# Performance work log

Measured on AMD Instinct MI355X. Metric: run time of the kernel, lower is better.

Reference implementation:

```python
import jax, jax.numpy as jnp
import numpy as np

GROUPS = 8
EPS = 1e-3  # keras GroupNormalization default epsilon


def group_norm(x, gamma, beta):
    # x: [B, H, W, C], channels-last, normalize over (H, W, C//G) per group
    B, H, W, C = x.shape
    g = x.reshape(B, H, W, GROUPS, C // GROUPS)
    mean = g.mean(axis=(1, 2, 4), keepdims=True)
    var = g.var(axis=(1, 2, 4), keepdims=True)
    g = (g - mean) * jax.lax.rsqrt(var + EPS)
    return g.reshape(B, H, W, C) * gamma + beta


def setup_inputs() -> dict:
    key = jax.random.key(0)
    ks = jax.random.split(key, 6)
    B, H, W, C = 4, 64, 64, 256
    s = 1.0 / np.sqrt(C)
    return {
        "x": jax.random.normal(ks[0], (B, H, W, C), jnp.float32),
        "gn_gamma": jnp.ones((C,), jnp.float32),
        "gn_beta": jnp.zeros((C,), jnp.float32),
        "Wq": jax.random.normal(ks[1], (C, C), jnp.float32) * s,
        "bq": jnp.zeros((C,), jnp.float32),
        "Wk": jax.random.normal(ks[2], (C, C), jnp.float32) * s,
        "bk": jnp.zeros((C,), jnp.float32),
        "Wv": jax.random.normal(ks[3], (C, C), jnp.float32) * s,
        "bv": jnp.zeros((C,), jnp.float32),
        "Wp": jax.random.normal(ks[4], (C, C), jnp.float32) * s,
        "bp": jnp.zeros((C,), jnp.float32),
    }


def reference(x, gn_gamma, gn_beta, Wq, bq, Wk, bk, Wv, bv, Wp, bp):
    B, H, W, C = x.shape
    scale = jnp.float32(C) ** -0.5
    xn = group_norm(x, gn_gamma, gn_beta)  # note: residual uses NORMALIZED input (as in source)
    xf = xn.reshape(B, H * W, C)           # flatten spatial -> [B, N, C]
    q = xf @ Wq + bq
    k = xf @ Wk + bk
    v = xf @ Wv + bv
    attn = jnp.einsum('bnc,bmc->bnm', q, k) * scale  # [B, N, N]
    attn = jax.nn.softmax(attn, axis=-1)
    out = jnp.einsum('bnm,bmc->bnc', attn, v)
    out = out @ Wp + bp
    return xn + out.reshape(B, H, W, C)
```

## Files before the change

kernel.cpp:

```cpp
#include <hip/hip_runtime.h>
#include <hip/hip_bf16.h>

typedef __bf16 bf16x8 __attribute__((ext_vector_type(8)));
typedef __bf16 bf16x4 __attribute__((ext_vector_type(4)));
typedef float f32x4 __attribute__((ext_vector_type(4)));
typedef float f32x16 __attribute__((ext_vector_type(16)));

#define MFMA16(a,b,c) __builtin_amdgcn_mfma_f32_16x16x32_bf16((a),(b),(c),0,0,0)
#define MFMA32(a,b,c) __builtin_amdgcn_mfma_f32_32x32x16_bf16((a),(b),(c),0,0,0)

__device__ __forceinline__ void gload_lds16(const void* g, void* l) {
    __builtin_amdgcn_global_load_lds((const __attribute__((address_space(1))) unsigned int*)g,
                                     (__attribute__((address_space(3))) unsigned int*)l, 16, 0, 0);
}

__global__ __launch_bounds__(256) void gn_stats1(const float* __restrict__ x,
                                                 float* __restrict__ pstats) {
    int blk = blockIdx.x;
    int bg = blk >> 4, sl = blk & 15;
    int b = bg >> 3, g = bg & 7;
    const float* base = x + ((size_t)b * 4096 + sl * 256) * 256 + g * 32;
    float s = 0.f, s2 = 0.f;
    for (int i = threadIdx.x; i < 2048; i += 256) {
        int pos = i >> 3, f4 = i & 7;
        float4 v = *(const float4*)(base + (size_t)pos * 256 + f4 * 4);
        s  += v.x + v.y + v.z + v.w;
        s2 += v.x * v.x + v.y * v.y + v.z * v.z + v.w * v.w;
    }
    for (int off = 32; off; off >>= 1) {
        s  += __shfl_down(s, off);
        s2 += __shfl_down(s2, off);
    }
    __shared__ float red[8];
    int wave = threadIdx.x >> 6, lane = threadIdx.x & 63;
    if (lane == 0) { red[wave] = s; red[4 + wave] = s2; }
    __syncthreads();
    if (threadIdx.x == 0) {
        pstats[blk * 2]     = red[0] + red[1] + red[2] + red[3];
        pstats[blk * 2 + 1] = red[4] + red[5] + red[6] + red[7];
    }
}

__global__ void gn_stats2(const float* __restrict__ pstats, float* __restrict__ stats) {
    int bg = threadIdx.x;
    if (bg < 32) {
        float S = 0.f, S2 = 0.f;
        for (int sl = 0; sl < 16; sl++) {
            S  += pstats[(bg * 16 + sl) * 2];
            S2 += pstats[(bg * 16 + sl) * 2 + 1];
        }
        const float invN = 1.f / 131072.f;
        float mean = S * invN;
        float var = S2 * invN - mean * mean;
        stats[bg * 2] = mean;
        stats[bg * 2 + 1] = rsqrtf(var + 1e-3f);
    }
}

__global__ __launch_bounds__(256) void gn_norm(const float* __restrict__ x,
                                               const float* __restrict__ gamma,
                                               const float* __restrict__ beta,
                                               const float* __restrict__ stats,
                                               float* __restrict__ xn_f32,
                                               __bf16* __restrict__ xn_bf) {
    size_t idx = (size_t)blockIdx.x * 256 + threadIdx.x;
    int c4 = (int)(idx & 63);
    int row = (int)(idx >> 6);
    int b = row >> 12;
    int g = c4 >> 3;
    float mean = stats[(b * 8 + g) * 2];
    float rstd = stats[(b * 8 + g) * 2 + 1];
    float4 xv = ((const float4*)x)[idx];
    float4 ga = ((const float4*)gamma)[c4];
    float4 be = ((const float4*)beta)[c4];
    float4 r;
    r.x = (xv.x - mean) * rstd * ga.x + be.x;
    r.y = (xv.y - mean) * rstd * ga.y + be.y;
    r.z = (xv.z - mean) * rstd * ga.z + be.z;
    r.w = (xv.w - mean) * rstd * ga.w + be.w;
    ((float4*)xn_f32)[idx] = r;
    bf16x4 o;
    o[0] = (__bf16)r.x; o[1] = (__bf16)r.y; o[2] = (__bf16)r.z; o[3] = (__bf16)r.w;
    *(bf16x4*)(xn_bf + idx * 4) = o;
}

__global__ __launch_bounds__(256) void prep_w(const float* __restrict__ Wq,
                                              const float* __restrict__ Wk,
                                              const float* __restrict__ Wv,
                                              const float* __restrict__ Wp,
                                              __bf16* __restrict__ wt) {
    int o = blockIdx.x * 256 + threadIdx.x;
    int w = o >> 16;
    int rem = o & 65535;
    int nt   = rem >> 12;
    int kf   = (rem >> 9) & 7;
    int quad = (rem >> 7) & 3;
    int l16  = (rem >> 3) & 15;
    int j    = rem & 7;
    int n = nt * 16 + l16;
    int k = kf * 32 + quad * 8 + j;
    const float* W = (w == 0) ? Wq : (w == 1) ? Wk : (w == 2) ? Wv : Wp;
    wt[o] = (__bf16)W[k * 256 + n];
}

__global__ __launch_bounds__(128, 2) void qkv_gemm(const __bf16* __restrict__ xn,
                                                   const __bf16* __restrict__ wt,
                                                   const float* __restrict__ bq,
                                                   const float* __restrict__ bk,
                                                   const float* __restrict__ bv,
                                                   __bf16* __restrict__ qout,
                                                   __bf16* __restrict__ kout,
                                                   __bf16* __restrict__ vtout) {
    __shared__ __bf16 atile[64][264];
    int w = blockIdx.z;
    const __bf16* Wl = wt + (size_t)w * 65536;
    int tid = threadIdx.x;
    int wave = tid >> 6, lane = tid & 63;
    int quad = lane >> 4, l16 = lane & 15;
    int m0 = blockIdx.x * 64;
    int ntbase = blockIdx.y * 8 + wave * 4;

#pragma unroll
    for (int i = 0; i < 16; i++) {
        int c = tid + 128 * i;
        int row = c >> 5, col = (c & 31) * 8;
        *(bf16x8*)&atile[row][col] = *(const bf16x8*)(xn + (size_t)(m0 + row) * 256 + col);
    }
    bf16x8 bfr[4][8];
#pragma unroll
    for (int ct = 0; ct < 4; ct++)
#pragma unroll
        for (int kf = 0; kf < 8; kf++)
            bfr[ct][kf] = *(const bf16x8*)(Wl + ((((size_t)(ntbase + ct) * 8 + kf) * 4 + quad) * 16 + l16) * 8);
    __syncthreads();

    f32x4 acc[4][4];
#pragma unroll
    for (int mt = 0; mt < 4; mt++)
#pragma unroll
        for (int ct = 0; ct < 4; ct++)
#pragma unroll
            for (int r = 0; r < 4; r++) acc[mt][ct][r] = 0.f;
#pragma unroll
    for (int kf = 0; kf < 8; kf++) {
        bf16x8 af[4];
#pragma unroll
        for (int mt = 0; mt < 4; mt++)
            af[mt] = *(const bf16x8*)&atile[mt * 16 + l16][kf * 32 + quad * 8];
#pragma unroll
        for (int mt = 0; mt < 4; mt++)
#pragma unroll
            for (int ct = 0; ct < 4; ct++)
                acc[mt][ct] = MFMA16(af[mt], bfr[ct][kf], acc[mt][ct]);
    }

    if (w == 2) {
        __syncthreads();
        __bf16 (*vtl)[70] = (__bf16(*)[70])atile;
#pragma unroll
        for (int mt = 0; mt < 4; mt++) {
#pragma unroll
            for (int ct = 0; ct < 4; ct++) {
                int cl = (wave * 4 + ct) * 16 + l16;
                float bias_v = bv[blockIdx.y * 128 + cl];
                bf16x4 pv;
#pragma unroll
                for (int r = 0; r < 4; r++) pv[r] = (__bf16)(acc[mt][ct][r] + bias_v);
                *(bf16x4*)&vtl[cl][mt * 16 + quad * 4] = pv;
            }
        }
        __syncthreads();
        int bb = m0 >> 12, n0g = m0 & 4095;
#pragma unroll
        for (int j = 0; j < 8; j++) {
            int chunk = tid + 128 * j;
            int cl = chunk >> 3, n8 = chunk & 7;
            *(bf16x8*)(vtout + ((size_t)(bb * 256 + blockIdx.y * 128 + cl)) * 4096 + n0g + n8 * 8)
                = *(const bf16x8*)&vtl[cl][n8 * 8];
        }
    } else {
        const float* bias = (w == 0) ? bq : bk;
        const float qscale = 0.09016844f;
#pragma unroll
        for (int mt = 0; mt < 4; mt++) {
#pragma unroll
            for (int ct = 0; ct < 4; ct++) {
                int c = (ntbase + ct) * 16 + l16;
                float bias_v = bias[c];
#pragma unroll
                for (int r = 0; r < 4; r++) {
                    int m = m0 + mt * 16 + quad * 4 + r;
                    float val = acc[mt][ct][r] + bias_v;
                    if (w == 0) qout[(size_t)m * 256 + c] = (__bf16)(val * qscale);
                    else        kout[(size_t)m * 256 + c] = (__bf16)val;
                }
            }
        }
    }
}

__global__ __launch_bounds__(256, 2) void flash_attn(const __bf16* __restrict__ q,
                                                     const __bf16* __restrict__ k,
                                                     const __bf16* __restrict__ vt,
                                                     __bf16* __restrict__ po,
                                                     float* __restrict__ ml) {
    __shared__ __align__(16) char smem[69632];
    __bf16 (*vtile0)[36] = (__bf16(*)[36])(smem + 32768);
    __bf16 (*vtile1)[36] = (__bf16(*)[36])(smem + 51200);
    __bf16 (*otr)[32][264] = (__bf16(*)[32][264])smem;

    const int tid = threadIdx.x;
    const int wave = tid >> 6, lane = tid & 63;
    const int l32 = lane & 31, h = lane >> 5;
    const int fid = blockIdx.x;
    const int cid = ((fid & 7) << 6) | (fid >> 3);
    const int qt  = cid & 31;
    const int ksb = cid >> 5;
    const int ks  = ksb & 3, b = ksb >> 2;
    const int row0 = qt * 128 + wave * 32;
    const size_t rowg0 = (size_t)b * 4096 + row0;

    const char*   kb = (const char*)(k + ((size_t)b * 4096 + ks * 1024) * 256);
    const __bf16* vb = vt + (size_t)b * 256 * 4096 + ks * 1024;

    int koff[4];
#pragma unroll
    for (int i = 0; i < 4; i++) {
        int P = wave * 256 + i * 64 + lane;
        int r = P >> 5, cp = P & 31;
        koff[i] = r * 512 + (cp ^ r) * 16;
    }
    const int kldsoff = wave * 4096;

    bf16x8 qf[16];
    const __bf16* qbase = q + (rowg0 + l32) * 256 + h * 8;
#pragma unroll
    for (int s = 0; s < 16; s++) qf[s] = *(const bf16x8*)(qbase + s * 16);

    f32x16 acc[8];
#pragma unroll
    for (int ct = 0; ct < 8; ct++)
#pragma unroll
        for (int r = 0; r < 16; r++) acc[ct][r] = 0.f;
    float mi = -1e30f, li = 0.f;

    const int vr_ = tid >> 2, vc4 = tid & 3;

#pragma unroll
    for (int i = 0; i < 4; i++)
        gload_lds16(kb + koff[i], smem + kldsoff + i * 1024);
    {
        bf16x8 vc[4];
#pragma unroll
        for (int i = 0; i < 4; i++)
            vc[i] = *(const bf16x8*)(vb + (size_t)(vr_ + 64 * i) * 4096 + vc4 * 8);
#pragma unroll
        for (int i = 0; i < 4; i++)
            *(bf16x8*)&vtile0[vr_ + 64 * i][vc4 * 8] = vc[i];
    }
    __syncthreads();

    for (int it = 0; it < 32; ++it) {
        const int cur = it & 1;
        char* kcur = smem + (cur ? 16384 : 0);
        char* knxt = smem + (cur ? 0 : 16384);
        __bf16 (*vcur)[36] = cur ? vtile1 : vtile0;
        __bf16 (*vnxt)[36] = cur ? vtile0 : vtile1;

        bf16x8 vc[4];
        if (it + 1 < 32) {
            const char* kg = kb + (size_t)(it + 1) * 16384;
#pragma unroll
            for (int i = 0; i < 4; i++)
                gload_lds16(kg + koff[i], knxt + kldsoff + i * 1024);
            const int kn = (it + 1) * 32;
#pragma unroll
            for (int i = 0; i < 4; i++)
                vc[i] = *(const bf16x8*)(vb + (size_t)(vr_ + 64 * i) * 4096 + kn + vc4 * 8);
        }

        f32x16 s;
#pragma unroll
        for (int r = 0; r < 16; r++) s[r] = 0.f;
#pragma unroll
        for (int kf = 0; kf < 16; kf++) {
            int cl = kf * 2 + h;
            bf16x8 ka = *(const bf16x8*)(kcur + l32 * 512 + ((cl ^ l32) << 4));
            s = MFMA32(ka, qf[kf], s);
        }
        float mx = s[0];
#pragma unroll
        for (int r = 1; r < 16; r++) mx = fmaxf(mx, s[r]);
        mx = fmaxf(mx, __shfl_xor(mx, 32));
        if (__ballot(mx > mi + 8.0f)) {
            float mnew = fmaxf(mi, mx);
            float alpha = exp2f(mi - mnew);
#pragma unroll
            for (int ct = 0; ct < 8; ct++)
#pragma unroll
                for (int r = 0; r < 16; r++) acc[ct][r] *= alpha;
            li *= alpha;
            mi = mnew;
        }
        float rs = 0.f;
#pragma unroll
        for (int r = 0; r < 16; r++) { float p = exp2f(s[r] - mi); s[r] = p; rs += p; }
        rs += __shfl_xor(rs, 32);
        li += rs;
        bf16x8 pf0, pf1;
#pragma unroll
        for (int j = 0; j < 8; j++) { pf0[j] = (__bf16)s[j]; pf1[j] = (__bf16)s[8 + j]; }
        if (it + 1 < 32) {
#pragma unroll
            for (int i = 0; i < 4; i++)
                *(bf16x8*)&vnxt[vr_ + 64 * i][vc4 * 8] = vc[i];
        }
#pragma unroll
        for (int ct = 0; ct < 8; ct++) {
            const __bf16* vr = &vcur[ct * 32 + l32][0];
            bf16x4 a00 = *(const bf16x4*)(vr + 4 * h);
            bf16x4 a01 = *(const bf16x4*)(vr + 8 + 4 * h);
            bf16x8 va0 = __builtin_shufflevector(a00, a01, 0, 1, 2, 3, 4, 5, 6, 7);
            acc[ct] = MFMA32(va0, pf0, acc[ct]);
            bf16x4 a10 = *(const bf16x4*)(vr + 16 + 4 * h);
            bf16x4 a11 = *(const bf16x4*)(vr + 24 + 4 * h);
            bf16x8 va1 = __builtin_shufflevector(a10, a11, 0, 1, 2, 3, 4, 5, 6, 7);
            acc[ct] = MFMA32(va1, pf1, acc[ct]);
        }
        __syncthreads();
    }

#pragma unroll
    for (int ct = 0; ct < 8; ct++) {
#pragma unroll
        for (int pk = 0; pk < 4; pk++) {
            bf16x4 op;
            op[0] = (__bf16)acc[ct][pk * 4];     op[1] = (__bf16)acc[ct][pk * 4 + 1];
            op[2] = (__bf16)acc[ct][pk * 4 + 2]; op[3] = (__bf16)acc[ct][pk * 4 + 3];
            *(bf16x4*)&otr[wave][l32][ct * 32 + pk * 8 + h * 4] = op;
        }
    }
    if (lane < 32) {
        float2 v; v.x = mi; v.y = li;
        *(float2*)&ml[((size_t)ks * 16384 + rowg0 + l32) * 2] = v;
    }
    __syncthreads();
    __bf16* pobase = po + ((size_t)ks * 16384 + rowg0) * 256;
    const int rr = lane >> 1, half = lane & 1;
#pragma unroll
    for (int j = 0; j < 16; j++) {
        bf16x8 val = *(const bf16x8*)&otr[wave][rr][half * 128 + j * 8];
        *(bf16x8*)(pobase + (size_t)rr * 256 + half * 128 + j * 8) = val;
    }
}

__global__ __launch_bounds__(128, 2) void proj_gemm(const __bf16* __restrict__ po,
                                                    const float* __restrict__ ml,
                                                    const __bf16* __restrict__ wpl,
                                                    const float* __restrict__ bp,
                                                    float* __restrict__ out) {
    __shared__ __bf16 atile[64][264];
    int tid = threadIdx.x;
    int wave = tid >> 6, lane = tid & 63;
    int quad = lane >> 4, l16 = lane & 15;
    int m0 = blockIdx.x * 64;
    int ntbase = blockIdx.y * 8 + wave * 4;

#pragma unroll
    for (int i = 0; i < 16; i++) {
        int c = tid + 128 * i;
        int row = c >> 5, col8 = c & 31;
        int m = m0 + row;
        float mm[4], ll[4];
#pragma unroll
        for (int s = 0; s < 4; s++) {
            float2 v = *(const float2*)&ml[((size_t)s * 16384 + m) * 2];
            mm[s] = v.x; ll[s] = v.y;
        }
        float M = fmaxf(fmaxf(mm[0], mm[1]), fmaxf(mm[2], mm[3]));
        float den = 0.f, w[4];
#pragma unroll
        for (int s = 0; s < 4; s++) { w[s] = exp2f(mm[s] - M); den += ll[s] * w[s]; }
        float accv[8];
#pragma unroll
        for (int e = 0; e < 8; e++) accv[e] = 0.f;
#pragma unroll
        for (int s = 0; s < 4; s++) {
            bf16x8 pv = *(const bf16x8*)(po + ((size_t)s * 16384 + m) * 256 + col8 * 8);
#pragma unroll
            for (int e = 0; e < 8; e++) accv[e] += w[s] * (float)pv[e];
        }
        float rinv = 1.f / den;
        bf16x8 o;
#pragma unroll
        for (int e = 0; e < 8; e++) o[e] = (__bf16)(accv[e] * rinv);
        *(bf16x8*)&atile[row][col8 * 8] = o;
    }
    bf16x8 bfr[4][8];
#pragma unroll
    for (int ct = 0; ct < 4; ct++)
#pragma unroll
        for (int kf = 0; kf < 8; kf++)
            bfr[ct][kf] = *(const bf16x8*)(wpl + ((((size_t)(ntbase + ct) * 8 + kf) * 4 + quad) * 16 + l16) * 8);
    __syncthreads();

    f32x4 acc[4][4];
#pragma unroll
    for (int mt = 0; mt < 4; mt++)
#pragma unroll
        for (int ct = 0; ct < 4; ct++)
#pragma unroll
            for (int r = 0; r < 4; r++) acc[mt][ct][r] = 0.f;
#pragma unroll
    for (int kf = 0; kf < 8; kf++) {
        bf16x8 af[4];
#pragma unroll
        for (int mt = 0; mt < 4; mt++)
            af[mt] = *(const bf16x8*)&atile[mt * 16 + l16][kf * 32 + quad * 8];
#pragma unroll
        for (int mt = 0; mt < 4; mt++)
#pragma unroll
            for (int ct = 0; ct < 4; ct++)
                acc[mt][ct] = MFMA16(af[mt], bfr[ct][kf], acc[mt][ct]);
    }
#pragma unroll
    for (int mt = 0; mt < 4; mt++) {
#pragma unroll
        for (int ct = 0; ct < 4; ct++) {
            int c = (ntbase + ct) * 16 + l16;
            float bias_v = bp[c];
#pragma unroll
            for (int r = 0; r < 4; r++) {
                int m = m0 + mt * 16 + quad * 4 + r;
                size_t idx = (size_t)m * 256 + c;
                out[idx] = out[idx] + acc[mt][ct][r] + bias_v;
            }
        }
    }
}

extern "C" void kernel_launch(void* const* d_in, const int* in_sizes, int n_in,
                              void* d_out, int out_size, void* d_ws, size_t ws_size,
                              hipStream_t stream) {
    const float* x     = (const float*)d_in[0];
    const float* gamma = (const float*)d_in[1];
    const float* beta  = (const float*)d_in[2];
    const float* Wq    = (const float*)d_in[3];
    const float* bq    = (const float*)d_in[4];
    const float* Wk    = (const float*)d_in[5];
    const float* bk    = (const float*)d_in[6];
    const float* Wv    = (const float*)d_in[7];
    const float* bv    = (const float*)d_in[8];
    const float* Wp    = (const float*)d_in[9];
    const float* bp    = (const float*)d_in[10];
    float* out = (float*)d_out;

    char* ws = (char*)d_ws;
    __bf16* xn_bf   = (__bf16*)(ws);
    __bf16* wt      = (__bf16*)(ws + 8388608);
    __bf16* qbuf    = (__bf16*)(ws + 8912896);
    __bf16* kbuf    = (__bf16*)(ws + 17301504);
    __bf16* vtbuf   = (__bf16*)(ws + 25690112);
    __bf16* po      = (__bf16*)(ws + 34078720);
    float*  ml      = (float*)(ws + 67633152);
    float*  pstats  = (float*)(ws + 68157440);
    float*  gstats  = (float*)(ws + 68161536);

    gn_stats1<<<512, 256, 0, stream>>>(x, pstats);
    gn_stats2<<<1, 64, 0, stream>>>(pstats, gstats);
    gn_norm<<<4096, 256, 0, stream>>>(x, gamma, beta, gstats, out, xn_bf);
    prep_w<<<1024, 256, 0, stream>>>(Wq, Wk, Wv, Wp, wt);
    qkv_gemm<<<dim3(256, 2, 3), 128, 0, stream>>>(xn_bf, wt, bq, bk, bv, qbuf, kbuf, vtbuf);
    flash_attn<<<512, 256, 0, stream>>>(qbuf, kbuf, vtbuf, po, ml);
    proj_gemm<<<dim3(256, 2), 128, 0, stream>>>(po, ml, wt + 3 * 65536, bp, out);
}
```

Before: 256.1 us.

## Software-pipeline QK^T one tile ahead of softmax/PV in flash attention loop

Restructures the attention main loop so the QK^T MFMAs for tile it+1 are issued before the softmax and PV of tile it, using two ping-pong score register sets and a K prefetch two tiles ahead. Uses explicit vmcnt/lgkmcnt waits with sched_barrier and raw s_barrier in place of __syncthreads, and raises wave priority around the PV MFMAs. It aims to hide MFMA and exp latency and global-load latency behind each other, at the cost of more live registers (extra score accumulators) and fragile hand-written wait counts.

```diff
diff --git a/kernel.cpp b/kernel.cpp
--- a/kernel.cpp
+++ b/kernel.cpp
@@ -245,90 +245,133 @@
     float mi = -1e30f, li = 0.f;
 
     const int vr_ = tid >> 2, vc4 = tid & 3;
+    bf16x8 vc[4];
 
 #pragma unroll
     for (int i = 0; i < 4; i++)
         gload_lds16(kb + koff[i], smem + kldsoff + i * 1024);
-    {
-        bf16x8 vc[4];
-#pragma unroll
-        for (int i = 0; i < 4; i++)
-            vc[i] = *(const bf16x8*)(vb + (size_t)(vr_ + 64 * i) * 4096 + vc4 * 8);
-#pragma unroll
-        for (int i = 0; i < 4; i++)
-            *(bf16x8*)&vtile0[vr_ + 64 * i][vc4 * 8] = vc[i];
-    }
-    __syncthreads();
-
-    for (int it = 0; it < 32; ++it) {
-        const int cur = it & 1;
-        char* kcur = smem + (cur ? 16384 : 0);
-        char* knxt = smem + (cur ? 0 : 16384);
-        __bf16 (*vcur)[36] = cur ? vtile1 : vtile0;
-        __bf16 (*vnxt)[36] = cur ? vtile0 : vtile1;
-
-        bf16x8 vc[4];
-        if (it + 1 < 32) {
-            const char* kg = kb + (size_t)(it + 1) * 16384;
-#pragma unroll
-            for (int i = 0; i < 4; i++)
-                gload_lds16(kg + koff[i], knxt + kldsoff + i * 1024);
-            const int kn = (it + 1) * 32;
-#pragma unroll
-            for (int i = 0; i < 4; i++)
-                vc[i] = *(const bf16x8*)(vb + (size_t)(vr_ + 64 * i) * 4096 + kn + vc4 * 8);
-        }
-
-        f32x16 s;
-#pragma unroll
-        for (int r = 0; r < 16; r++) s[r] = 0.f;
-#pragma unroll
-        for (int kf = 0; kf < 16; kf++) {
-            int cl = kf * 2 + h;
-            bf16x8 ka = *(const bf16x8*)(kcur + l32 * 512 + ((cl ^ l32) << 4));
-            s = MFMA32(ka, qf[kf], s);
-        }
-        float mx = s[0];
-#pragma unroll
-        for (int r = 1; r < 16; r++) mx = fmaxf(mx, s[r]);
-        mx = fmaxf(mx, __shfl_xor(mx, 32));
-        if (__ballot(mx > mi + 8.0f)) {
-            float mnew = fmaxf(mi, mx);
-            float alpha = exp2f(mi - mnew);
-#pragma unroll
-            for (int ct = 0; ct < 8; ct++)
-#pragma unroll
-                for (int r = 0; r < 16; r++) acc[ct][r] *= alpha;
-            li *= alpha;
-            mi = mnew;
-        }
-        float rs = 0.f;
-#pragma unroll
-        for (int r = 0; r < 16; r++) { float p = exp2f(s[r] - mi); s[r] = p; rs += p; }
-        rs += __shfl_xor(rs, 32);
-        li += rs;
-        bf16x8 pf0, pf1;
-#pragma unroll
-        for (int j = 0; j < 8; j++) { pf0[j] = (__bf16)s[j]; pf1[j] = (__bf16)s[8 + j]; }
-        if (it + 1 < 32) {
-#pragma unroll
-            for (int i = 0; i < 4; i++)
-                *(bf16x8*)&vnxt[vr_ + 64 * i][vc4 * 8] = vc[i];
-        }
-#pragma unroll
-        for (int ct = 0; ct < 8; ct++) {
-            const __bf16* vr = &vcur[ct * 32 + l32][0];
-            bf16x4 a00 = *(const bf16x4*)(vr + 4 * h);
-            bf16x4 a01 = *(const bf16x4*)(vr + 8 + 4 * h);
-            bf16x8 va0 = __builtin_shufflevector(a00, a01, 0, 1, 2, 3, 4, 5, 6, 7);
-            acc[ct] = MFMA32(va0, pf0, acc[ct]);
-            bf16x4 a10 = *(const bf16x4*)(vr + 16 + 4 * h);
-            bf16x4 a11 = *(const bf16x4*)(vr + 24 + 4 * h);
-            bf16x8 va1 = __builtin_shufflevector(a10, a11, 0, 1, 2, 3, 4, 5, 6, 7);
-            acc[ct] = MFMA32(va1, pf1, acc[ct]);
-        }
-        __syncthreads();
-    }
+#pragma unroll
+    for (int i = 0; i < 4; i++)
+        vc[i] = *(const bf16x8*)(vb + (size_t)(vr_ + 64 * i) * 4096 + vc4 * 8);
+    asm volatile("s_waitcnt vmcnt(4)" ::: "memory");
+    __builtin_amdgcn_sched_barrier(0);
+    __builtin_amdgcn_s_barrier();
+
+    f32x16 sA0, sA1, sB0, sB1;
+#pragma unroll
+    for (int r = 0; r < 16; r++) { sA0[r] = 0.f; sA1[r] = 0.f; }
+#pragma unroll
+    for (int kf = 0; kf < 8; kf++) {
+        int cl = kf * 2 + h;
+        bf16x8 ka = *(const bf16x8*)(smem + l32 * 512 + ((cl ^ l32) << 4));
+        sA0 = MFMA32(ka, qf[kf], sA0);
+    }
+#pragma unroll
+    for (int kf = 8; kf < 16; kf++) {
+        int cl = kf * 2 + h;
+        bf16x8 ka = *(const bf16x8*)(smem + l32 * 512 + ((cl ^ l32) << 4));
+        sA1 = MFMA32(ka, qf[kf], sA1);
+    }
+#pragma unroll
+    for (int i = 0; i < 4; i++)
+        *(bf16x8*)&vtile0[vr_ + 64 * i][vc4 * 8] = vc[i];
+#pragma unroll
+    for (int i = 0; i < 4; i++)
+        gload_lds16(kb + 16384 + koff[i], smem + 16384 + kldsoff + i * 1024);
+#pragma unroll
+    for (int i = 0; i < 4; i++)
+        vc[i] = *(const bf16x8*)(vb + (size_t)(vr_ + 64 * i) * 4096 + 32 + vc4 * 8);
+    asm volatile("s_waitcnt vmcnt(4) lgkmcnt(0)" ::: "memory");
+    __builtin_amdgcn_sched_barrier(0);
+    __builtin_amdgcn_s_barrier();
+
+#define FA_BODY(IT, PAR, SC0, SC1, SN0, SN1)                                        \
+  {                                                                                 \
+    const int it_ = (IT);                                                           \
+    \
+    if (it_ < 30) {                                                                 \
+      const char* kg_ = kb + (size_t)(it_ + 2) * 16384;                             \
+      char* kw_ = smem + ((PAR) ? 16384 : 0);                                       \
+      _Pragma("unroll") for (int i = 0; i < 4; i++)                                 \
+        gload_lds16(kg_ + koff[i], kw_ + kldsoff + i * 1024);                       \
+    }                                                                               \
+                      \
+    if (it_ < 31) {                                                                 \
+      const char* kr_ = smem + ((PAR) ? 0 : 16384);                                 \
+      _Pragma("unroll") for (int r = 0; r < 16; r++) { SN0[r] = 0.f; SN1[r] = 0.f; }\
+      _Pragma("unroll") for (int kf = 0; kf < 8; kf++) {                            \
+        int cl = kf * 2 + h;                                                        \
+        bf16x8 ka = *(const bf16x8*)(kr_ + l32 * 512 + ((cl ^ l32) << 4));          \
+        SN0 = MFMA32(ka, qf[kf], SN0);                                              \
+      }                                                                             \
+      _Pragma("unroll") for (int kf = 8; kf < 16; kf++) {                           \
+        int cl = kf * 2 + h;                                                        \
+        bf16x8 ka = *(const bf16x8*)(kr_ + l32 * 512 + ((cl ^ l32) << 4));          \
+        SN1 = MFMA32(ka, qf[kf], SN1);                                              \
+      }                                                                             \
+    }                                                                               \
+             \
+    f32x16 s_;                                                                      \
+    _Pragma("unroll") for (int r = 0; r < 16; r++) s_[r] = SC0[r] + SC1[r];         \
+    float mx = s_[0];                                                               \
+    _Pragma("unroll") for (int r = 1; r < 16; r++) mx = fmaxf(mx, s_[r]);           \
+    mx = fmaxf(mx, __shfl_xor(mx, 32));                                             \
+    if (__ballot(mx > mi + 8.0f)) {                                                 \
+      float mnew = fmaxf(mi, mx);                                                   \
+      float alpha = exp2f(mi - mnew);                                               \
+      _Pragma("unroll") for (int ct = 0; ct < 8; ct++)                              \
+        _Pragma("unroll") for (int r = 0; r < 16; r++) acc[ct][r] *= alpha;         \
+      li *= alpha;                                                                  \
+      mi = mnew;                                                                    \
+    }                                                                               \
+    float rs = 0.f;                                                                 \
+    _Pragma("unroll") for (int r = 0; r < 16; r++) {                                \
+      float p = exp2f(s_[r] - mi); s_[r] = p; rs += p; }                            \
+    rs += __shfl_xor(rs, 32);                                                       \
+    li += rs;                                                                       \
+    bf16x8 pf0, pf1;                                                                \
+    _Pragma("unroll") for (int j = 0; j < 8; j++) {                                 \
+      pf0[j] = (__bf16)s_[j]; pf1[j] = (__bf16)s_[8 + j]; }                         \
+              \
+    if (it_ < 31) {                                                                 \
+      __bf16 (*vn_)[36] = (PAR) ? vtile0 : vtile1;                                  \
+      _Pragma("unroll") for (int i = 0; i < 4; i++)                                 \
+        *(bf16x8*)&vn_[vr_ + 64 * i][vc4 * 8] = vc[i];                              \
+    }                                                                               \
+        \
+    if (it_ < 30) {                                                                 \
+      const int kn_ = (it_ + 2) * 32;                                               \
+      _Pragma("unroll") for (int i = 0; i < 4; i++)                                 \
+        vc[i] = *(const bf16x8*)(vb + (size_t)(vr_ + 64 * i) * 4096 + kn_ + vc4 * 8);\
+    }                                                                               \
+                                                         \
+    {                                                                               \
+      __bf16 (*vc_)[36] = (PAR) ? vtile1 : vtile0;                                  \
+      __builtin_amdgcn_s_setprio(1);                                                \
+      _Pragma("unroll") for (int ct = 0; ct < 8; ct++) {                            \
+        const __bf16* vr2 = &vc_[ct * 32 + l32][0];                                 \
+        bf16x4 a00 = *(const bf16x4*)(vr2 + 4 * h);                                 \
+        bf16x4 a01 = *(const bf16x4*)(vr2 + 8 + 4 * h);                             \
+        bf16x8 va0 = __builtin_shufflevector(a00, a01, 0, 1, 2, 3, 4, 5, 6, 7);     \
+        acc[ct] = MFMA32(va0, pf0, acc[ct]);                                        \
+        bf16x4 a10 = *(const bf16x4*)(vr2 + 16 + 4 * h);                            \
+        bf16x4 a11 = *(const bf16x4*)(vr2 + 24 + 4 * h);                            \
+        bf16x8 va1 = __builtin_shufflevector(a10, a11, 0, 1, 2, 3, 4, 5, 6, 7);     \
+        acc[ct] = MFMA32(va1, pf1, acc[ct]);                                        \
+      }                                                                             \
+      __builtin_amdgcn_s_setprio(0);                                                \
+    }                                                                               \
+             \
+    asm volatile("s_waitcnt vmcnt(4) lgkmcnt(0)" ::: "memory");                     \
+    __builtin_amdgcn_sched_barrier(0);                                              \
+    __builtin_amdgcn_s_barrier();                                                   \
+  }
+
+    for (int i2 = 0; i2 < 16; ++i2) {
+        FA_BODY(2 * i2,     0, sA0, sA1, sB0, sB1);
+        FA_BODY(2 * i2 + 1, 1, sB0, sB1, sA0, sA1);
+    }
+#undef FA_BODY
 
 #pragma unroll
     for (int ct = 0; ct < 8; ct++) {
```

Result: slower. 399.6 us (+56.0%).

## Software-pipeline flash attention loop, overlapping QK^T of next tile with PV

Applied to the files above, without the earlier changes.

Restructures the attention main loop so that the QK^T MFMAs for tile it are interleaved with the PV MFMAs for tile it-1, using a peeled prologue and epilogue and a manually unrolled two-phase macro body. Explicit s_waitcnt with partial vmcnt plus raw s_barrier replace __syncthreads, so global K/V prefetch can stay in flight across iterations, and s_setprio raises priority around the MFMA block. The aim is to hide softmax latency and memory waits behind matrix work. In exchange it adds register pressure from carrying the previous tile's probabilities, and its correctness depends on hand-counted vmcnt values.

```diff
diff --git a/kernel.cpp b/kernel.cpp
--- a/kernel.cpp
+++ b/kernel.cpp
@@ -245,90 +245,145 @@
     float mi = -1e30f, li = 0.f;
 
     const int vr_ = tid >> 2, vc4 = tid & 3;
+    bf16x8 vc[4];
+    bf16x8 pf0, pf1;
 
 #pragma unroll
     for (int i = 0; i < 4; i++)
         gload_lds16(kb + koff[i], smem + kldsoff + i * 1024);
+#pragma unroll
+    for (int i = 0; i < 4; i++)
+        vc[i] = *(const bf16x8*)(vb + (size_t)(vr_ + 64 * i) * 4096 + vc4 * 8);
+#pragma unroll
+    for (int i = 0; i < 4; i++)
+        gload_lds16(kb + 16384 + koff[i], smem + 16384 + kldsoff + i * 1024);
+    asm volatile("s_waitcnt vmcnt(8)" ::: "memory");
+    __builtin_amdgcn_sched_barrier(0);
+    __builtin_amdgcn_s_barrier();
+
     {
-        bf16x8 vc[4];
-#pragma unroll
-        for (int i = 0; i < 4; i++)
-            vc[i] = *(const bf16x8*)(vb + (size_t)(vr_ + 64 * i) * 4096 + vc4 * 8);
+        f32x16 s_;
+#pragma unroll
+        for (int r = 0; r < 16; r++) s_[r] = 0.f;
+#pragma unroll
+        for (int kf = 0; kf < 16; kf++) {
+            int cl = kf * 2 + h;
+            bf16x8 ka = *(const bf16x8*)(smem + l32 * 512 + ((cl ^ l32) << 4));
+            s_ = MFMA32(ka, qf[kf], s_);
+        }
+        float mx = s_[0];
+#pragma unroll
+        for (int r = 1; r < 16; r++) mx = fmaxf(mx, s_[r]);
+        mx = fmaxf(mx, __shfl_xor(mx, 32));
+        mi = mx;
+        float rs = 0.f;
+#pragma unroll
+        for (int r = 0; r < 16; r++) { float p = exp2f(s_[r] - mi); s_[r] = p; rs += p; }
+        rs += __shfl_xor(rs, 32);
+        li = rs;
+#pragma unroll
+        for (int j = 0; j < 8; j++) { pf0[j] = (__bf16)s_[j]; pf1[j] = (__bf16)s_[8 + j]; }
 #pragma unroll
         for (int i = 0; i < 4; i++)
             *(bf16x8*)&vtile0[vr_ + 64 * i][vc4 * 8] = vc[i];
+#pragma unroll
+        for (int i = 0; i < 4; i++)
+            vc[i] = *(const bf16x8*)(vb + (size_t)(vr_ + 64 * i) * 4096 + 32 + vc4 * 8);
+    }
+    asm volatile("s_waitcnt vmcnt(4) lgkmcnt(0)" ::: "memory");
+    __builtin_amdgcn_sched_barrier(0);
+    __builtin_amdgcn_s_barrier();
+
+#define FA_BODY(IT, PAR, STAGE)                                                     \
+  {                                                                                 \
+    const int it_ = (IT);                                                           \
+            \
+    { __bf16 (*vw_)[36] = (PAR) ? vtile1 : vtile0;                                  \
+      _Pragma("unroll") for (int i = 0; i < 4; i++)                                 \
+        *(bf16x8*)&vw_[vr_ + 64 * i][vc4 * 8] = vc[i]; }                            \
+                      \
+    if (STAGE) {                                                                    \
+      const char* kg_ = kb + (size_t)(it_ + 1) * 16384;                             \
+      char* kw_ = smem + ((PAR) ? 0 : 16384);                                       \
+      _Pragma("unroll") for (int i = 0; i < 4; i++)                                 \
+        gload_lds16(kg_ + koff[i], kw_ + kldsoff + i * 1024);                       \
+                \
+      const int kn_ = (it_ + 1) * 32;                                               \
+      _Pragma("unroll") for (int i = 0; i < 4; i++)                                 \
+        vc[i] = *(const bf16x8*)(vb + (size_t)(vr_ + 64 * i) * 4096 + kn_ + vc4 * 8);\
+    }                                                                               \
+             \
+    {                                                                               \
+      const char* kr_ = smem + ((PAR) ? 16384 : 0);                                 \
+      __bf16 (*vp_)[36] = (PAR) ? vtile0 : vtile1;                                  \
+      f32x16 s_;                                                                    \
+      _Pragma("unroll") for (int r = 0; r < 16; r++) s_[r] = 0.f;                   \
+      __builtin_amdgcn_s_setprio(1);                                                \
+      _Pragma("unroll") for (int u = 0; u < 8; u++) {                               \
+        { int cl = (2 * u) * 2 + h;                                                 \
+          bf16x8 ka = *(const bf16x8*)(kr_ + l32 * 512 + ((cl ^ l32) << 4));        \
+          s_ = MFMA32(ka, qf[2 * u], s_); }                                         \
+        { int cl = (2 * u + 1) * 2 + h;                                             \
+          bf16x8 ka = *(const bf16x8*)(kr_ + l32 * 512 + ((cl ^ l32) << 4));        \
+          s_ = MFMA32(ka, qf[2 * u + 1], s_); }                                     \
+        { const __bf16* vr2 = &vp_[u * 32 + l32][0];                                \
+          bf16x4 a00 = *(const bf16x4*)(vr2 + 4 * h);                               \
+          bf16x4 a01 = *(const bf16x4*)(vr2 + 8 + 4 * h);                           \
+          bf16x8 va0 = __builtin_shufflevector(a00, a01, 0, 1, 2, 3, 4, 5, 6, 7);   \
+          acc[u] = MFMA32(va0, pf0, acc[u]);                                        \
+          bf16x4 a10 = *(const bf16x4*)(vr2 + 16 + 4 * h);                          \
+          bf16x4 a11 = *(const bf16x4*)(vr2 + 24 + 4 * h);                          \
+          bf16x8 va1 = __builtin_shufflevector(a10, a11, 0, 1, 2, 3, 4, 5, 6, 7);   \
+          acc[u] = MFMA32(va1, pf1, acc[u]);                                        \
+        }                                                                           \
+      }                                                                             \
+      __builtin_amdgcn_s_setprio(0);                                                \
+                  \
+      float mx = s_[0];                                                             \
+      _Pragma("unroll") for (int r = 1; r < 16; r++) mx = fmaxf(mx, s_[r]);         \
+      mx = fmaxf(mx, __shfl_xor(mx, 32));                                           \
+      if (__ballot(mx > mi + 8.0f)) {                                               \
+        float mnew = fmaxf(mi, mx);                                                 \
+        float alpha = exp2f(mi - mnew);                                             \
+        _Pragma("unroll") for (int ct = 0; ct < 8; ct++)                            \
+          _Pragma("unroll") for (int r = 0; r < 16; r++) acc[ct][r] *= alpha;       \
+        li *= alpha; mi = mnew;                                                     \
+      }                                                                             \
+      float rs = 0.f;                                                               \
+      _Pragma("unroll") for (int r = 0; r < 16; r++) {                              \
+        float p = exp2f(s_[r] - mi); s_[r] = p; rs += p; }                          \
+      rs += __shfl_xor(rs, 32);                                                     \
+      li += rs;                                                                     \
+      _Pragma("unroll") for (int j = 0; j < 8; j++) {                               \
+        pf0[j] = (__bf16)s_[j]; pf1[j] = (__bf16)s_[8 + j]; }                       \
+    }                                                                               \
+             \
+    if (STAGE) { asm volatile("s_waitcnt vmcnt(4) lgkmcnt(0)" ::: "memory"); }      \
+    else       { asm volatile("s_waitcnt lgkmcnt(0)" ::: "memory"); }               \
+    __builtin_amdgcn_sched_barrier(0);                                              \
+    __builtin_amdgcn_s_barrier();                                                   \
+  }
+
+    for (int i2 = 0; i2 < 15; ++i2) {
+        FA_BODY(2 * i2 + 1, 1, 1);
+        FA_BODY(2 * i2 + 2, 0, 1);
+    }
+    FA_BODY(31, 1, 0);
+#undef FA_BODY
+
+#pragma unroll
+    for (int u = 0; u < 8; u++) {
+        const __bf16* vr2 = &vtile1[u * 32 + l32][0];
+        bf16x4 a00 = *(const bf16x4*)(vr2 + 4 * h);
+        bf16x4 a01 = *(const bf16x4*)(vr2 + 8 + 4 * h);
+        bf16x8 va0 = __builtin_shufflevector(a00, a01, 0, 1, 2, 3, 4, 5, 6, 7);
+        acc[u] = MFMA32(va0, pf0, acc[u]);
+        bf16x4 a10 = *(const bf16x4*)(vr2 + 16 + 4 * h);
+        bf16x4 a11 = *(const bf16x4*)(vr2 + 24 + 4 * h);
+        bf16x8 va1 = __builtin_shufflevector(a10, a11, 0, 1, 2, 3, 4, 5, 6, 7);
+        acc[u] = MFMA32(va1, pf1, acc[u]);
     }
     __syncthreads();
-
-    for (int it = 0; it < 32; ++it) {
-        const int cur = it & 1;
-        char* kcur = smem + (cur ? 16384 : 0);
-        char* knxt = smem + (cur ? 0 : 16384);
-        __bf16 (*vcur)[36] = cur ? vtile1 : vtile0;
-        __bf16 (*vnxt)[36] = cur ? vtile0 : vtile1;
-
-        bf16x8 vc[4];
-        if (it + 1 < 32) {
-            const char* kg = kb + (size_t)(it + 1) * 16384;
-#pragma unroll
-            for (int i = 0; i < 4; i++)
-                gload_lds16(kg + koff[i], knxt + kldsoff + i * 1024);
-            const int kn = (it + 1) * 32;
-#pragma unroll
-            for (int i = 0; i < 4; i++)
-                vc[i] = *(const bf16x8*)(vb + (size_t)(vr_ + 64 * i) * 4096 + kn + vc4 * 8);
-        }
-
-        f32x16 s;
-#pragma unroll
-        for (int r = 0; r < 16; r++) s[r] = 0.f;
-#pragma unroll
-        for (int kf = 0; kf < 16; kf++) {
-            int cl = kf * 2 + h;
-            bf16x8 ka = *(const bf16x8*)(kcur + l32 * 512 + ((cl ^ l32) << 4));
-            s = MFMA32(ka, qf[kf], s);
-        }
-        float mx = s[0];
-#pragma unroll
-        for (int r = 1; r < 16; r++) mx = fmaxf(mx, s[r]);
-        mx = fmaxf(mx, __shfl_xor(mx, 32));
-        if (__ballot(mx > mi + 8.0f)) {
-            float mnew = fmaxf(mi, mx);
-            float alpha = exp2f(mi - mnew);
-#pragma unroll
-            for (int ct = 0; ct < 8; ct++)
-#pragma unroll
-                for (int r = 0; r < 16; r++) acc[ct][r] *= alpha;
-            li *= alpha;
-            mi = mnew;
-        }
-        float rs = 0.f;
-#pragma unroll
-        for (int r = 0; r < 16; r++) { float p = exp2f(s[r] - mi); s[r] = p; rs += p; }
-        rs += __shfl_xor(rs, 32);
-        li += rs;
-        bf16x8 pf0, pf1;
-#pragma unroll
-        for (int j = 0; j < 8; j++) { pf0[j] = (__bf16)s[j]; pf1[j] = (__bf16)s[8 + j]; }
-        if (it + 1 < 32) {
-#pragma unroll
-            for (int i = 0; i < 4; i++)
-                *(bf16x8*)&vnxt[vr_ + 64 * i][vc4 * 8] = vc[i];
-        }
-#pragma unroll
-        for (int ct = 0; ct < 8; ct++) {
-            const __bf16* vr = &vcur[ct * 32 + l32][0];
-            bf16x4 a00 = *(const bf16x4*)(vr + 4 * h);
-            bf16x4 a01 = *(const bf16x4*)(vr + 8 + 4 * h);
-            bf16x8 va0 = __builtin_shufflevector(a00, a01, 0, 1, 2, 3, 4, 5, 6, 7);
-            acc[ct] = MFMA32(va0, pf0, acc[ct]);
-            bf16x4 a10 = *(const bf16x4*)(vr + 16 + 4 * h);
-            bf16x4 a11 = *(const bf16x4*)(vr + 24 + 4 * h);
-            bf16x8 va1 = __builtin_shufflevector(a10, a11, 0, 1, 2, 3, 4, 5, 6, 7);
-            acc[ct] = MFMA32(va1, pf1, acc[ct]);
-        }
-        __syncthreads();
-    }
 
 #pragma unroll
     for (int ct = 0; ct < 8; ct++) {
```

New measurement: 273.0 us. 1.07x slower.

## Load V tiles directly into LDS with swizzled layout and split QK accumulators

Applied to the files above, without the earlier changes.

V tiles now go from global memory straight into LDS through global_load_lds with an XOR-swizzled, unpadded layout, replacing the register round-trip and padded stores. The V reads in the PV MFMA loop follow the new swizzle. The QK^T product is split into two independent accumulator chains to shorten the MFMA dependency chain. The PV loop is also wrapped in s_setprio. This trims VGPR use and LDS store instructions, at the cost of an explicit vmcnt wait before each barrier, which exposes global load latency at the end of every iteration.

```diff
diff --git a/kernel.cpp b/kernel.cpp
--- a/kernel.cpp
+++ b/kernel.cpp
@@ -205,8 +205,6 @@
                                                      __bf16* __restrict__ po,
                                                      float* __restrict__ ml) {
     __shared__ __align__(16) char smem[69632];
-    __bf16 (*vtile0)[36] = (__bf16(*)[36])(smem + 32768);
-    __bf16 (*vtile1)[36] = (__bf16(*)[36])(smem + 51200);
     __bf16 (*otr)[32][264] = (__bf16(*)[32][264])smem;
 
     const int tid = threadIdx.x;
@@ -232,6 +230,16 @@
     }
     const int kldsoff = wave * 4096;
 
+    const int r4 = (lane >> 2) & 15, c4v = lane & 3;
+    const int swl = (r4 ^ (r4 >> 2)) & 3;
+    int voff[4];
+#pragma unroll
+    for (int i = 0; i < 4; i++) {
+        int ch = wave * 64 + i * 16 + r4;
+        voff[i] = ch * 4096 + (c4v ^ swl) * 8;
+    }
+    const int vldsoff = wave * 4096;
+
     bf16x8 qf[16];
     const __bf16* qbase = q + (rowg0 + l32) * 256 + h * 8;
 #pragma unroll
@@ -244,53 +252,55 @@
         for (int r = 0; r < 16; r++) acc[ct][r] = 0.f;
     float mi = -1e30f, li = 0.f;
 
-    const int vr_ = tid >> 2, vc4 = tid & 3;
-
 #pragma unroll
     for (int i = 0; i < 4; i++)
         gload_lds16(kb + koff[i], smem + kldsoff + i * 1024);
-    {
-        bf16x8 vc[4];
-#pragma unroll
-        for (int i = 0; i < 4; i++)
-            vc[i] = *(const bf16x8*)(vb + (size_t)(vr_ + 64 * i) * 4096 + vc4 * 8);
-#pragma unroll
-        for (int i = 0; i < 4; i++)
-            *(bf16x8*)&vtile0[vr_ + 64 * i][vc4 * 8] = vc[i];
-    }
-    __syncthreads();
+#pragma unroll
+    for (int i = 0; i < 4; i++)
+        gload_lds16(vb + voff[i], smem + 32768 + vldsoff + i * 1024);
+    asm volatile("s_waitcnt vmcnt(0)" ::: "memory");
+    __builtin_amdgcn_sched_barrier(0);
+    __builtin_amdgcn_s_barrier();
 
     for (int it = 0; it < 32; ++it) {
         const int cur = it & 1;
-        char* kcur = smem + (cur ? 16384 : 0);
-        char* knxt = smem + (cur ? 0 : 16384);
-        __bf16 (*vcur)[36] = cur ? vtile1 : vtile0;
-        __bf16 (*vnxt)[36] = cur ? vtile0 : vtile1;
-
-        bf16x8 vc[4];
+        const char* kcur = smem + (cur ? 16384 : 0);
+        const char* vcur = smem + 32768 + (cur ? 16384 : 0);
+
         if (it + 1 < 32) {
             const char* kg = kb + (size_t)(it + 1) * 16384;
+            char* kw = smem + (cur ? 0 : 16384);
 #pragma unroll
             for (int i = 0; i < 4; i++)
-                gload_lds16(kg + koff[i], knxt + kldsoff + i * 1024);
+                gload_lds16(kg + koff[i], kw + kldsoff + i * 1024);
             const int kn = (it + 1) * 32;
+            char* vw = smem + 32768 + (cur ? 0 : 16384);
 #pragma unroll
             for (int i = 0; i < 4; i++)
-                vc[i] = *(const bf16x8*)(vb + (size_t)(vr_ + 64 * i) * 4096 + kn + vc4 * 8);
-        }
-
-        f32x16 s;
-#pragma unroll
-        for (int r = 0; r < 16; r++) s[r] = 0.f;
-#pragma unroll
-        for (int kf = 0; kf < 16; kf++) {
-            int cl = kf * 2 + h;
-            bf16x8 ka = *(const bf16x8*)(kcur + l32 * 512 + ((cl ^ l32) << 4));
-            s = MFMA32(ka, qf[kf], s);
-        }
-        float mx = s[0];
-#pragma unroll
-        for (int r = 1; r < 16; r++) mx = fmaxf(mx, s[r]);
+                gload_lds16(vb + voff[i] + kn, vw + vldsoff + i * 1024);
+        }
+
+        f32x16 s0_, s1_;
+#pragma unroll
+        for (int r = 0; r < 16; r++) { s0_[r] = 0.f; s1_[r] = 0.f; }
+#pragma unroll
+        for (int u = 0; u < 8; u++) {
+            {
+                int cl = 2 * u + h;
+                bf16x8 ka = *(const bf16x8*)(kcur + l32 * 512 + ((cl ^ l32) << 4));
+                s0_ = MFMA32(ka, qf[u], s0_);
+            }
+            {
+                int cl = 2 * (u + 8) + h;
+                bf16x8 ka = *(const bf16x8*)(kcur + l32 * 512 + ((cl ^ l32) << 4));
+                s1_ = MFMA32(ka, qf[u + 8], s1_);
+            }
+        }
+#pragma unroll
+        for (int r = 0; r < 16; r++) s0_[r] += s1_[r];
+        float mx = s0_[0];
+#pragma unroll
+        for (int r = 1; r < 16; r++) mx = fmaxf(mx, s0_[r]);
         mx = fmaxf(mx, __shfl_xor(mx, 32));
         if (__ballot(mx > mi + 8.0f)) {
             float mnew = fmaxf(mi, mx);
@@ -304,30 +314,35 @@
         }
         float rs = 0.f;
 #pragma unroll
-        for (int r = 0; r < 16; r++) { float p = exp2f(s[r] - mi); s[r] = p; rs += p; }
+        for (int r = 0; r < 16; r++) { float p = exp2f(s0_[r] - mi); s0_[r] = p; rs += p; }
         rs += __shfl_xor(rs, 32);
         li += rs;
         bf16x8 pf0, pf1;
 #pragma unroll
-        for (int j = 0; j < 8; j++) { pf0[j] = (__bf16)s[j]; pf1[j] = (__bf16)s[8 + j]; }
-        if (it + 1 < 32) {
-#pragma unroll
-            for (int i = 0; i < 4; i++)
-                *(bf16x8*)&vnxt[vr_ + 64 * i][vc4 * 8] = vc[i];
-        }
-#pragma unroll
-        for (int ct = 0; ct < 8; ct++) {
-            const __bf16* vr = &vcur[ct * 32 + l32][0];
-            bf16x4 a00 = *(const bf16x4*)(vr + 4 * h);
-            bf16x4 a01 = *(const bf16x4*)(vr + 8 + 4 * h);
-            bf16x8 va0 = __builtin_shufflevector(a00, a01, 0, 1, 2, 3, 4, 5, 6, 7);
-            acc[ct] = MFMA32(va0, pf0, acc[ct]);
-            bf16x4 a10 = *(const bf16x4*)(vr + 16 + 4 * h);
-            bf16x4 a11 = *(const bf16x4*)(vr + 24 + 4 * h);
-            bf16x8 va1 = __builtin_shufflevector(a10, a11, 0, 1, 2, 3, 4, 5, 6, 7);
-            acc[ct] = MFMA32(va1, pf1, acc[ct]);
-        }
-        __syncthreads();
+        for (int j = 0; j < 8; j++) { pf0[j] = (__bf16)s0_[j]; pf1[j] = (__bf16)s0_[8 + j]; }
+
+        {
+            const int sb = ((l32 ^ (l32 >> 2)) & 3) << 4;
+            const char* vrow = vcur + l32 * 64 + h * 8;
+            __builtin_amdgcn_s_setprio(1);
+#pragma unroll
+            for (int ct = 0; ct < 8; ct++) {
+                const char* vr2 = vrow + ct * 2048;
+                bf16x4 a00 = *(const bf16x4*)(vr2 + sb);
+                bf16x4 a01 = *(const bf16x4*)(vr2 + (sb ^ 16));
+                bf16x8 va0 = __builtin_shufflevector(a00, a01, 0, 1, 2, 3, 4, 5, 6, 7);
+                acc[ct] = MFMA32(va0, pf0, acc[ct]);
+                bf16x4 a10 = *(const bf16x4*)(vr2 + (sb ^ 32));
+                bf16x4 a11 = *(const bf16x4*)(vr2 + (sb ^ 48));
+                bf16x8 va1 = __builtin_shufflevector(a10, a11, 0, 1, 2, 3, 4, 5, 6, 7);
+                acc[ct] = MFMA32(va1, pf1, acc[ct]);
+            }
+            __builtin_amdgcn_s_setprio(0);
+        }
+
+        asm volatile("s_waitcnt vmcnt(0) lgkmcnt(0)" ::: "memory");
+        __builtin_amdgcn_sched_barrier(0);
+        __builtin_amdgcn_s_barrier();
     }
 
 #pragma unroll
```

Result: no change. 255.9 us (-0.1%).
